# Kernel optimization log

Measured on AMD Instinct MI355X. Metric: run time of the kernel, lower is better.

The kernel has to match this reference:

```python
import jax, jax.numpy as jnp
import numpy as np

B, SQ, SKV, D = 16, 2048, 2048, 128


def setup_inputs() -> dict:
    key = jax.random.key(0)
    kq, kk, kv = jax.random.split(key, 3)
    q = jax.random.normal(kq, (B, SQ, D), dtype=jnp.float32)
    k = jax.random.normal(kk, (B, SKV, D), dtype=jnp.float32)
    v = jax.random.normal(kv, (B, SKV, D), dtype=jnp.float32)
    return {"q": q, "k": k, "v": v, "dropout_p": 0}


def reference(q, k, v, dropout_p):
    # scores = q @ k^T, scaled by 1/sqrt(d)
    scale = 1.0 / np.sqrt(q.shape[-1]).astype(np.float32)
    scores = jnp.einsum('bqd,bkd->bqk', q, k) * scale  # [B, SQ, SKV]
    attn = jax.nn.softmax(scores, axis=-1)
    # dropout with p=dropout_p (0 here -> identity; deterministic baseline)
    if dropout_p > 0:
        keep = 1.0 - dropout_p
        mask = jax.random.bernoulli(jax.random.key(42), keep, attn.shape)
        attn = jnp.where(mask, attn / keep, 0.0)
    return jnp.einsum('bqk,bkd->bqd', attn, v)
```

## Files before the change

kernel.cpp:

```cpp
#include <hip/hip_runtime.h>
#include <hip/hip_bf16.h>
#include <cstdint>
#include <cmath>

#define SQL 2048
#define SKVL 2048
#define DD 128
#define NB 16
#define QBLK 64
#define KVB 64
#define NT (SKVL / KVB)

typedef __attribute__((ext_vector_type(8))) short short8;
typedef __attribute__((ext_vector_type(4))) float f32x4;

__device__ __forceinline__ ushort f2bf(float x) {
    union { float f; uint32_t u; } v; v.f = x;
    uint32_t r = v.u + 0x7FFFu + ((v.u >> 16) & 1u);
    return (ushort)(r >> 16);
}

__global__ void convert_scale_k(const float* __restrict__ in, ushort* __restrict__ out, float scale) {
    size_t i = (size_t)blockIdx.x * blockDim.x + threadIdx.x;
    const f32x4* p = (const f32x4*)in + i * 2;
    f32x4 a = p[0], b = p[1];
    short8 o;
    o[0] = (short)f2bf(a[0] * scale);
    o[1] = (short)f2bf(a[1] * scale);
    o[2] = (short)f2bf(a[2] * scale);
    o[3] = (short)f2bf(a[3] * scale);
    o[4] = (short)f2bf(b[0] * scale);
    o[5] = (short)f2bf(b[1] * scale);
    o[6] = (short)f2bf(b[2] * scale);
    o[7] = (short)f2bf(b[3] * scale);
    *((short8*)out + i) = o;
}

__global__ void convert_k_tiled(const float* __restrict__ in, ushort* __restrict__ out) {
    int gid = blockIdx.x * blockDim.x + threadIdx.x;
    int c16 = gid & 15;
    int rg  = gid >> 4;
    int r   = rg & 63;
    int tile = rg >> 6;
    const f32x4* p = (const f32x4*)(in + (size_t)rg * DD + c16 * 8);
    f32x4 a = p[0], b = p[1];
    short8 o;
    o[0] = (short)f2bf(a[0]); o[1] = (short)f2bf(a[1]);
    o[2] = (short)f2bf(a[2]); o[3] = (short)f2bf(a[3]);
    o[4] = (short)f2bf(b[0]); o[5] = (short)f2bf(b[1]);
    o[6] = (short)f2bf(b[2]); o[7] = (short)f2bf(b[3]);
    int cs = c16 ^ (r & 7);
    *(short8*)(out + ((size_t)tile << 13) + r * 128 + cs * 8) = o;
}

__global__ void convert_vt_tiled(const float* __restrict__ v, ushort* __restrict__ vt) {
    __shared__ float tile[64][129];
    int bid = blockIdx.x;
    int kt = bid & 31;
    int b  = bid >> 5;
    int tx = threadIdx.x & 63, ty = threadIdx.x >> 6;
    const float* src = v + ((size_t)b * SKVL + (size_t)kt * 64) * DD;
#pragma unroll
    for (int r = ty; r < 64; r += 4) {
        tile[r][tx * 2]     = src[(size_t)r * DD + tx * 2];
        tile[r][tx * 2 + 1] = src[(size_t)r * DD + tx * 2 + 1];
    }
    __syncthreads();
    ushort* dst = vt + ((size_t)bid << 13);
#pragma unroll
    for (int i = 0; i < 4; ++i) {
        int q = threadIdx.x + 256 * i;
        int d = q >> 3;
        int csp = q & 7;
        int cs = csp ^ (d & 7);
        int h = cs >> 2, g = cs & 3;
        short8 o;
#pragma unroll
        for (int j = 0; j < 8; ++j) {
            int kv = h * 32 + g * 4 + (j & 3) + 16 * (j >> 2);
            o[j] = (short)f2bf(tile[kv][d]);
        }
        *(short8*)(dst + d * 64 + csp * 8) = o;
    }
}

#define GLD_LDS16(gsrc, ldst) \
    __builtin_amdgcn_global_load_lds((const __attribute__((address_space(1))) uint32_t*)(gsrc), \
                                     (__attribute__((address_space(3))) uint32_t*)(ldst), 16, 0, 0)

__global__ __launch_bounds__(256, 2) void fattn(
    const ushort* __restrict__ qb, const ushort* __restrict__ kbt,
    const ushort* __restrict__ vbt, float* __restrict__ out)
{
    __shared__ short8 kls[2][1024];
    __shared__ short8 vls[2][1024];

    int bid = blockIdx.x;
    int swz = (bid & 7) * 64 + (bid >> 3);
    int b  = swz >> 5;
    int qt = swz & 31;
    int lane = threadIdx.x & 63;
    int w = threadIdx.x >> 6;
    int g = lane >> 4;
    int qi = lane & 15;
    int rx = qi & 7;
    int qrow = qt * QBLK + w * 16 + qi;

    const ushort* ktile0 = kbt + ((size_t)(b * NT) << 13);
    const ushort* vtile0 = vbt + ((size_t)(b * NT) << 13);

    const ushort* qptr = qb + ((size_t)b * SQL + qrow) * DD;
    short8 qf[4];
#pragma unroll
    for (int ks = 0; ks < 4; ++ks)
        qf[ks] = *(const short8*)(qptr + ks * 32 + g * 8);

    f32x4 acc[8];
#pragma unroll
    for (int i = 0; i < 8; ++i) acc[i] = (f32x4)0.f;
    float m = -1e30f, lsum = 0.f;

#pragma unroll
    for (int i = 0; i < 4; ++i) {
        int off = w * 4096 + i * 1024;
        GLD_LDS16((const char*)ktile0 + off + lane * 16, (char*)&kls[0][0] + off);
        GLD_LDS16((const char*)vtile0 + off + lane * 16, (char*)&vls[0][0] + off);
    }
    __syncthreads();

    for (int t = 0; t < NT; ++t) {
        int cur = t & 1, nxt = cur ^ 1;
        if (t + 1 < NT) {
            const char* ks = (const char*)ktile0 + ((size_t)(t + 1) << 14);
            const char* vs = (const char*)vtile0 + ((size_t)(t + 1) << 14);
#pragma unroll
            for (int i = 0; i < 4; ++i) {
                int off = w * 4096 + i * 1024;
                GLD_LDS16(ks + off + lane * 16, (char*)&kls[nxt][0] + off);
                GLD_LDS16(vs + off + lane * 16, (char*)&vls[nxt][0] + off);
            }
        }
        f32x4 st[4];
        __builtin_amdgcn_s_setprio(1);
#pragma unroll
        for (int sub = 0; sub < 4; ++sub) {
            f32x4 s = (f32x4)0.f;
            int r = sub * 16 + qi;
#pragma unroll
            for (int ks = 0; ks < 4; ++ks) {
                short8 kf = kls[cur][r * 16 + ((ks * 4 + g) ^ rx)];
                s = __builtin_amdgcn_mfma_f32_16x16x32_bf16(kf, qf[ks], s, 0, 0, 0);
            }
            st[sub] = s;
        }
        __builtin_amdgcn_s_setprio(0);
        float m0 = fmaxf(fmaxf(st[0][0], st[0][1]), fmaxf(st[0][2], st[0][3]));
        float m1 = fmaxf(fmaxf(st[1][0], st[1][1]), fmaxf(st[1][2], st[1][3]));
        float m2 = fmaxf(fmaxf(st[2][0], st[2][1]), fmaxf(st[2][2], st[2][3]));
        float m3 = fmaxf(fmaxf(st[3][0], st[3][1]), fmaxf(st[3][2], st[3][3]));
        float tmax = fmaxf(fmaxf(m0, m1), fmaxf(m2, m3));
        tmax = fmaxf(tmax, __shfl_xor(tmax, 16));
        tmax = fmaxf(tmax, __shfl_xor(tmax, 32));
        if (!__all(tmax - m <= 11.5f)) {
            float mnew = fmaxf(m, tmax);
            float alpha = exp2f(m - mnew);
            m = mnew;
            lsum *= alpha;
#pragma unroll
            for (int i = 0; i < 8; ++i) {
                acc[i][0] *= alpha; acc[i][1] *= alpha;
                acc[i][2] *= alpha; acc[i][3] *= alpha;
            }
        }
        float pv[16];
        float ps[4];
#pragma unroll
        for (int s = 0; s < 4; ++s) {
            pv[s * 4 + 0] = exp2f(st[s][0] - m);
            pv[s * 4 + 1] = exp2f(st[s][1] - m);
            pv[s * 4 + 2] = exp2f(st[s][2] - m);
            pv[s * 4 + 3] = exp2f(st[s][3] - m);
            ps[s] = (pv[s * 4 + 0] + pv[s * 4 + 1]) + (pv[s * 4 + 2] + pv[s * 4 + 3]);
        }
        lsum += (ps[0] + ps[1]) + (ps[2] + ps[3]);
        union { short8 v; uint32_t u[4]; } P0, P1;
#pragma unroll
        for (int i = 0; i < 4; ++i) {
            asm("v_cvt_pk_bf16_f32 %0, %1, %2" : "=v"(P0.u[i]) : "v"(pv[2 * i]), "v"(pv[2 * i + 1]));
            asm("v_cvt_pk_bf16_f32 %0, %1, %2" : "=v"(P1.u[i]) : "v"(pv[8 + 2 * i]), "v"(pv[8 + 2 * i + 1]));
        }
        __builtin_amdgcn_s_setprio(1);
#pragma unroll
        for (int dt = 0; dt < 8; ++dt) {
            int d = dt * 16 + qi;
            acc[dt] = __builtin_amdgcn_mfma_f32_16x16x32_bf16(
                vls[cur][d * 8 + (g ^ rx)], P0.v, acc[dt], 0, 0, 0);
            acc[dt] = __builtin_amdgcn_mfma_f32_16x16x32_bf16(
                vls[cur][d * 8 + ((4 + g) ^ rx)], P1.v, acc[dt], 0, 0, 0);
        }
        __builtin_amdgcn_s_setprio(0);
        __syncthreads();
    }

    lsum += __shfl_xor(lsum, 16);
    lsum += __shfl_xor(lsum, 32);
    float inv = 1.f / lsum;
    float* optr = out + ((size_t)b * SQL + qrow) * DD + g * 4;
#pragma unroll
    for (int dt = 0; dt < 8; ++dt) {
        f32x4 o;
        o[0] = acc[dt][0] * inv; o[1] = acc[dt][1] * inv;
        o[2] = acc[dt][2] * inv; o[3] = acc[dt][3] * inv;
        *(f32x4*)(optr + dt * 16) = o;
    }
}

extern "C" void kernel_launch(void* const* d_in, const int* in_sizes, int n_in,
                              void* d_out, int out_size, void* d_ws, size_t ws_size,
                              hipStream_t stream) {
    const float* q = (const float*)d_in[0];
    const float* k = (const float*)d_in[1];
    const float* v = (const float*)d_in[2];
    float* out = (float*)d_out;

    uint8_t* w = (uint8_t*)d_ws;
    size_t tsz = (size_t)NB * SQL * DD * sizeof(ushort);
    ushort* qb  = (ushort*)w;
    ushort* kbt = (ushort*)(w + tsz);
    ushort* vbt = (ushort*)(w + 2 * tsz);

    float qscale = 1.4426950408889634f / sqrtf((float)DD);
    int n8 = NB * SQL * DD / 8;
    convert_scale_k<<<n8 / 256, 256, 0, stream>>>(q, qb, qscale);
    convert_k_tiled<<<NB * SKVL * 16 / 256, 256, 0, stream>>>(k, kbt);
    convert_vt_tiled<<<NB * (SKVL / 64), 256, 0, stream>>>(v, vbt);
    fattn<<<NB * (SQL / QBLK), 256, 0, stream>>>(qb, kbt, vbt, out);
}
```

Baseline: 160.3 us.

## Halve Q and KV tile sizes to 32 with two-wave blocks

Shrinks the attention tiles from 64 to 32 query rows and 32 keys per step, with 128-thread blocks. The K and V pre-conversion kernels are rewritten to emit 32-row swizzled tiles, and the P·V product becomes a single MFMA per output tile. The online-softmax rescale check now tests each lane's max with a wave vote and only does the cross-lane reduction when a rescale is needed. This doubles the block count and cuts per-block LDS use, aiming at more blocks in flight. The cost is half the K/V reuse per loaded tile, twice as many barrier-separated iterations, and more L2 traffic.

```diff
diff --git a/kernel.cpp b/kernel.cpp
--- a/kernel.cpp
+++ b/kernel.cpp
@@ -7,8 +7,8 @@
 #define SKVL 2048
 #define DD 128
 #define NB 16
-#define QBLK 64
-#define KVB 64
+#define QBLK 32
+#define KVB 32
 #define NT (SKVL / KVB)
 
 typedef __attribute__((ext_vector_type(8))) short short8;
@@ -40,8 +40,8 @@
     int gid = blockIdx.x * blockDim.x + threadIdx.x;
     int c16 = gid & 15;
     int rg  = gid >> 4;
-    int r   = rg & 63;
-    int tile = rg >> 6;
+    int r   = rg & 31;
+    int tile = rg >> 5;
     const f32x4* p = (const f32x4*)(in + (size_t)rg * DD + c16 * 8);
     f32x4 a = p[0], b = p[1];
     short8 o;
@@ -50,37 +50,36 @@
     o[4] = (short)f2bf(b[0]); o[5] = (short)f2bf(b[1]);
     o[6] = (short)f2bf(b[2]); o[7] = (short)f2bf(b[3]);
     int cs = c16 ^ (r & 7);
-    *(short8*)(out + ((size_t)tile << 13) + r * 128 + cs * 8) = o;
+    *(short8*)(out + ((size_t)tile << 12) + r * 128 + cs * 8) = o;
 }
 
 __global__ void convert_vt_tiled(const float* __restrict__ v, ushort* __restrict__ vt) {
-    __shared__ float tile[64][129];
+    __shared__ float tile[32][129];
     int bid = blockIdx.x;
-    int kt = bid & 31;
-    int b  = bid >> 5;
-    int tx = threadIdx.x & 63, ty = threadIdx.x >> 6;
-    const float* src = v + ((size_t)b * SKVL + (size_t)kt * 64) * DD;
-#pragma unroll
-    for (int r = ty; r < 64; r += 4) {
-        tile[r][tx * 2]     = src[(size_t)r * DD + tx * 2];
-        tile[r][tx * 2 + 1] = src[(size_t)r * DD + tx * 2 + 1];
+    int kt = bid & 63;
+    int b  = bid >> 6;
+    int tx = threadIdx.x;
+    const float* src = v + ((size_t)b * SKVL + (size_t)kt * 32) * DD;
+#pragma unroll
+    for (int i = 0; i < 16; ++i) {
+        int e = i * 256 + tx;
+        tile[e >> 7][e & 127] = src[e];
     }
     __syncthreads();
-    ushort* dst = vt + ((size_t)bid << 13);
-#pragma unroll
-    for (int i = 0; i < 4; ++i) {
-        int q = threadIdx.x + 256 * i;
-        int d = q >> 3;
-        int csp = q & 7;
-        int cs = csp ^ (d & 7);
-        int h = cs >> 2, g = cs & 3;
+    ushort* dst = vt + ((size_t)bid << 12);
+#pragma unroll
+    for (int i = 0; i < 2; ++i) {
+        int q = i * 256 + tx;
+        int d = q >> 2;
+        int csp = q & 3;
+        int cs = csp ^ ((d >> 1) & 3);
         short8 o;
 #pragma unroll
         for (int j = 0; j < 8; ++j) {
-            int kv = h * 32 + g * 4 + (j & 3) + 16 * (j >> 2);
+            int kv = (j >> 2) * 16 + cs * 4 + (j & 3);
             o[j] = (short)f2bf(tile[kv][d]);
         }
-        *(short8*)(dst + d * 64 + csp * 8) = o;
+        *(short8*)(dst + d * 32 + csp * 8) = o;
     }
 }
 
@@ -88,26 +87,27 @@
     __builtin_amdgcn_global_load_lds((const __attribute__((address_space(1))) uint32_t*)(gsrc), \
                                      (__attribute__((address_space(3))) uint32_t*)(ldst), 16, 0, 0)
 
-__global__ __launch_bounds__(256, 2) void fattn(
+__global__ __launch_bounds__(128, 2) void fattn(
     const ushort* __restrict__ qb, const ushort* __restrict__ kbt,
     const ushort* __restrict__ vbt, float* __restrict__ out)
 {
-    __shared__ short8 kls[2][1024];
-    __shared__ short8 vls[2][1024];
+    __shared__ short8 kls[2][512];
+    __shared__ short8 vls[2][512];
 
     int bid = blockIdx.x;
-    int swz = (bid & 7) * 64 + (bid >> 3);
-    int b  = swz >> 5;
-    int qt = swz & 31;
+    int swz = (bid & 7) * 128 + (bid >> 3);
+    int b  = swz >> 6;
+    int qt = swz & 63;
     int lane = threadIdx.x & 63;
     int w = threadIdx.x >> 6;
     int g = lane >> 4;
     int qi = lane & 15;
     int rx = qi & 7;
+    int vx = g ^ ((qi >> 1) & 3);
     int qrow = qt * QBLK + w * 16 + qi;
 
-    const ushort* ktile0 = kbt + ((size_t)(b * NT) << 13);
-    const ushort* vtile0 = vbt + ((size_t)(b * NT) << 13);
+    const ushort* ktile0 = kbt + ((size_t)(b * NT) << 12);
+    const ushort* vtile0 = vbt + ((size_t)(b * NT) << 12);
 
     const ushort* qptr = qb + ((size_t)b * SQL + qrow) * DD;
     short8 qf[4];
@@ -131,8 +131,8 @@
     for (int t = 0; t < NT; ++t) {
         int cur = t & 1, nxt = cur ^ 1;
         if (t + 1 < NT) {
-            const char* ks = (const char*)ktile0 + ((size_t)(t + 1) << 14);
-            const char* vs = (const char*)vtile0 + ((size_t)(t + 1) << 14);
+            const char* ks = (const char*)ktile0 + ((size_t)(t + 1) << 13);
+            const char* vs = (const char*)vtile0 + ((size_t)(t + 1) << 13);
 #pragma unroll
             for (int i = 0; i < 4; ++i) {
                 int off = w * 4096 + i * 1024;
@@ -140,10 +140,10 @@
                 GLD_LDS16(vs + off + lane * 16, (char*)&vls[nxt][0] + off);
             }
         }
-        f32x4 st[4];
+        f32x4 st[2];
         __builtin_amdgcn_s_setprio(1);
 #pragma unroll
-        for (int sub = 0; sub < 4; ++sub) {
+        for (int sub = 0; sub < 2; ++sub) {
             f32x4 s = (f32x4)0.f;
             int r = sub * 16 + qi;
 #pragma unroll
@@ -156,12 +156,10 @@
         __builtin_amdgcn_s_setprio(0);
         float m0 = fmaxf(fmaxf(st[0][0], st[0][1]), fmaxf(st[0][2], st[0][3]));
         float m1 = fmaxf(fmaxf(st[1][0], st[1][1]), fmaxf(st[1][2], st[1][3]));
-        float m2 = fmaxf(fmaxf(st[2][0], st[2][1]), fmaxf(st[2][2], st[2][3]));
-        float m3 = fmaxf(fmaxf(st[3][0], st[3][1]), fmaxf(st[3][2], st[3][3]));
-        float tmax = fmaxf(fmaxf(m0, m1), fmaxf(m2, m3));
-        tmax = fmaxf(tmax, __shfl_xor(tmax, 16));
-        tmax = fmaxf(tmax, __shfl_xor(tmax, 32));
-        if (!__all(tmax - m <= 11.5f)) {
+        float vmax = fmaxf(m0, m1);
+        if (__any(vmax > m + 11.5f)) {
+            float tmax = fmaxf(vmax, __shfl_xor(vmax, 16));
+            tmax = fmaxf(tmax, __shfl_xor(tmax, 32));
             float mnew = fmaxf(m, tmax);
             float alpha = exp2f(m - mnew);
             m = mnew;
@@ -172,31 +170,25 @@
                 acc[i][2] *= alpha; acc[i][3] *= alpha;
             }
         }
-        float pv[16];
-        float ps[4];
-#pragma unroll
-        for (int s = 0; s < 4; ++s) {
+        float pv[8];
+#pragma unroll
+        for (int s = 0; s < 2; ++s) {
             pv[s * 4 + 0] = exp2f(st[s][0] - m);
             pv[s * 4 + 1] = exp2f(st[s][1] - m);
             pv[s * 4 + 2] = exp2f(st[s][2] - m);
             pv[s * 4 + 3] = exp2f(st[s][3] - m);
-            ps[s] = (pv[s * 4 + 0] + pv[s * 4 + 1]) + (pv[s * 4 + 2] + pv[s * 4 + 3]);
-        }
-        lsum += (ps[0] + ps[1]) + (ps[2] + ps[3]);
-        union { short8 v; uint32_t u[4]; } P0, P1;
-#pragma unroll
-        for (int i = 0; i < 4; ++i) {
-            asm("v_cvt_pk_bf16_f32 %0, %1, %2" : "=v"(P0.u[i]) : "v"(pv[2 * i]), "v"(pv[2 * i + 1]));
-            asm("v_cvt_pk_bf16_f32 %0, %1, %2" : "=v"(P1.u[i]) : "v"(pv[8 + 2 * i]), "v"(pv[8 + 2 * i + 1]));
-        }
+        }
+        lsum += ((pv[0] + pv[1]) + (pv[2] + pv[3])) + ((pv[4] + pv[5]) + (pv[6] + pv[7]));
+        union { short8 v; uint32_t u[4]; } P;
+#pragma unroll
+        for (int i = 0; i < 4; ++i)
+            asm("v_cvt_pk_bf16_f32 %0, %1, %2" : "=v"(P.u[i]) : "v"(pv[2 * i]), "v"(pv[2 * i + 1]));
         __builtin_amdgcn_s_setprio(1);
 #pragma unroll
         for (int dt = 0; dt < 8; ++dt) {
             int d = dt * 16 + qi;
             acc[dt] = __builtin_amdgcn_mfma_f32_16x16x32_bf16(
-                vls[cur][d * 8 + (g ^ rx)], P0.v, acc[dt], 0, 0, 0);
-            acc[dt] = __builtin_amdgcn_mfma_f32_16x16x32_bf16(
-                vls[cur][d * 8 + ((4 + g) ^ rx)], P1.v, acc[dt], 0, 0, 0);
+                vls[cur][d * 4 + vx], P.v, acc[dt], 0, 0, 0);
         }
         __builtin_amdgcn_s_setprio(0);
         __syncthreads();
@@ -233,6 +225,6 @@
     int n8 = NB * SQL * DD / 8;
     convert_scale_k<<<n8 / 256, 256, 0, stream>>>(q, qb, qscale);
     convert_k_tiled<<<NB * SKVL * 16 / 256, 256, 0, stream>>>(k, kbt);
-    convert_vt_tiled<<<NB * (SKVL / 64), 256, 0, stream>>>(v, vbt);
-    fattn<<<NB * (SQL / QBLK), 256, 0, stream>>>(qb, kbt, vbt, out);
-}
+    convert_vt_tiled<<<NB * (SKVL / 32), 256, 0, stream>>>(v, vbt);
+    fattn<<<NB * (SQL / QBLK), 128, 0, stream>>>(qb, kbt, vbt, out);
+}
```

Result: slower. 164.2 us (+2.4%).

## Load V fragments directly from global into registers, bypassing LDS

Applied to the files above, without the earlier changes.

Removes the V double-buffer in shared memory and has each lane load its V^T fragments straight from global memory into registers at the start of each KV tile. The V^T pre-conversion drops its XOR swizzle, since no LDS bank conflicts apply any more. The online-softmax rescale check now runs a cheap per-lane any() test before the cross-lane max shuffles. This halves LDS use and the async LDS copies, but adds 16 global loads of 16 bytes per lane per iteration, which may stall the PV MFMAs and raise register pressure.

```diff
diff --git a/kernel.cpp b/kernel.cpp
--- a/kernel.cpp
+++ b/kernel.cpp
@@ -71,8 +71,7 @@
     for (int i = 0; i < 4; ++i) {
         int q = threadIdx.x + 256 * i;
         int d = q >> 3;
-        int csp = q & 7;
-        int cs = csp ^ (d & 7);
+        int cs = q & 7;
         int h = cs >> 2, g = cs & 3;
         short8 o;
 #pragma unroll
@@ -80,7 +79,7 @@
             int kv = h * 32 + g * 4 + (j & 3) + 16 * (j >> 2);
             o[j] = (short)f2bf(tile[kv][d]);
         }
-        *(short8*)(dst + d * 64 + csp * 8) = o;
+        *(short8*)(dst + d * 64 + cs * 8) = o;
     }
 }
 
@@ -93,7 +92,6 @@
     const ushort* __restrict__ vbt, float* __restrict__ out)
 {
     __shared__ short8 kls[2][1024];
-    __shared__ short8 vls[2][1024];
 
     int bid = blockIdx.x;
     int swz = (bid & 7) * 64 + (bid >> 3);
@@ -107,7 +105,7 @@
     int qrow = qt * QBLK + w * 16 + qi;
 
     const ushort* ktile0 = kbt + ((size_t)(b * NT) << 13);
-    const ushort* vtile0 = vbt + ((size_t)(b * NT) << 13);
+    const short8* vlp = (const short8*)vbt + ((size_t)(b * NT) << 10) + qi * 8 + g;
 
     const ushort* qptr = qb + ((size_t)b * SQL + qrow) * DD;
     short8 qf[4];
@@ -124,20 +122,24 @@
     for (int i = 0; i < 4; ++i) {
         int off = w * 4096 + i * 1024;
         GLD_LDS16((const char*)ktile0 + off + lane * 16, (char*)&kls[0][0] + off);
-        GLD_LDS16((const char*)vtile0 + off + lane * 16, (char*)&vls[0][0] + off);
     }
     __syncthreads();
 
     for (int t = 0; t < NT; ++t) {
         int cur = t & 1, nxt = cur ^ 1;
+        short8 vf[16];
+#pragma unroll
+        for (int dt = 0; dt < 8; ++dt) {
+#pragma unroll
+            for (int h = 0; h < 2; ++h)
+                vf[dt * 2 + h] = vlp[t * 1024 + dt * 128 + h * 4];
+        }
         if (t + 1 < NT) {
             const char* ks = (const char*)ktile0 + ((size_t)(t + 1) << 14);
-            const char* vs = (const char*)vtile0 + ((size_t)(t + 1) << 14);
 #pragma unroll
             for (int i = 0; i < 4; ++i) {
                 int off = w * 4096 + i * 1024;
                 GLD_LDS16(ks + off + lane * 16, (char*)&kls[nxt][0] + off);
-                GLD_LDS16(vs + off + lane * 16, (char*)&vls[nxt][0] + off);
             }
         }
         f32x4 st[4];
@@ -158,10 +160,10 @@
         float m1 = fmaxf(fmaxf(st[1][0], st[1][1]), fmaxf(st[1][2], st[1][3]));
         float m2 = fmaxf(fmaxf(st[2][0], st[2][1]), fmaxf(st[2][2], st[2][3]));
         float m3 = fmaxf(fmaxf(st[3][0], st[3][1]), fmaxf(st[3][2], st[3][3]));
-        float tmax = fmaxf(fmaxf(m0, m1), fmaxf(m2, m3));
-        tmax = fmaxf(tmax, __shfl_xor(tmax, 16));
-        tmax = fmaxf(tmax, __shfl_xor(tmax, 32));
-        if (!__all(tmax - m <= 11.5f)) {
+        float vmax = fmaxf(fmaxf(m0, m1), fmaxf(m2, m3));
+        if (__any(vmax > m + 11.5f)) {
+            float tmax = fmaxf(vmax, __shfl_xor(vmax, 16));
+            tmax = fmaxf(tmax, __shfl_xor(tmax, 32));
             float mnew = fmaxf(m, tmax);
             float alpha = exp2f(m - mnew);
             m = mnew;
@@ -192,11 +194,8 @@
         __builtin_amdgcn_s_setprio(1);
 #pragma unroll
         for (int dt = 0; dt < 8; ++dt) {
-            int d = dt * 16 + qi;
-            acc[dt] = __builtin_amdgcn_mfma_f32_16x16x32_bf16(
-                vls[cur][d * 8 + (g ^ rx)], P0.v, acc[dt], 0, 0, 0);
-            acc[dt] = __builtin_amdgcn_mfma_f32_16x16x32_bf16(
-                vls[cur][d * 8 + ((4 + g) ^ rx)], P1.v, acc[dt], 0, 0, 0);
+            acc[dt] = __builtin_amdgcn_mfma_f32_16x16x32_bf16(vf[dt * 2 + 0], P0.v, acc[dt], 0, 0, 0);
+            acc[dt] = __builtin_amdgcn_mfma_f32_16x16x32_bf16(vf[dt * 2 + 1], P1.v, acc[dt], 0, 0, 0);
         }
         __builtin_amdgcn_s_setprio(0);
         __syncthreads();
```

New measurement: 234.3 us. 1.46x slower.
